# Performance work log

Hardware: AMD Instinct MI355X
Metric: run time of the kernel (lower is better)

Reference implementation:

```python
import jax, jax.numpy as jnp
import numpy as np

N_NODES = 50000
N_EDGES = 600000
H_DIM = 128
BN_EPS = 1e-5


def setup_inputs() -> dict:
    key = jax.random.key(0)
    k1, k2, k3, k4 = jax.random.split(key, 4)
    ent_emb = jax.random.normal(k1, (N_NODES, H_DIM), dtype=jnp.float32)
    # xavier_normal_ init for the 128x128 weight
    std = float(np.sqrt(2.0 / (H_DIM + H_DIM)))
    neigh_w = jax.random.normal(k2, (H_DIM, H_DIM), dtype=jnp.float32) * std
    gamma = jnp.ones((H_DIM,), dtype=jnp.float32)
    beta = jnp.zeros((H_DIM,), dtype=jnp.float32)
    src = jax.random.randint(k3, (N_EDGES,), 0, N_NODES, dtype=jnp.int32)
    dst = jax.random.randint(k4, (N_EDGES,), 0, N_NODES, dtype=jnp.int32)
    return {"ent_emb": ent_emb, "neigh_w": neigh_w, "gamma": gamma,
            "beta": beta, "src": src, "dst": dst}


def reference(ent_emb, neigh_w, gamma, beta, src, dst):
    # Edge dot-product scores: u_dot_v('emb','emb')  -> [E]
    e_src = ent_emb[src]                      # [E, H]
    e_dst = ent_emb[dst]                      # [E, H]
    scores = jnp.sum(e_src * e_dst, axis=-1)  # [E]

    # edge_softmax: softmax over incoming edges of each destination node
    seg_max = jax.ops.segment_max(scores, dst, num_segments=N_NODES)
    seg_max = jnp.where(jnp.isfinite(seg_max), seg_max, 0.0)  # nodes w/o edges
    e = jnp.exp(scores - seg_max[dst])                         # [E]
    seg_sum = jax.ops.segment_sum(e, dst, num_segments=N_NODES)
    norm = e / seg_sum[dst]                                    # [E]

    # update_all(u_mul_e, sum): weighted gather-sum aggregation
    msg = e_src * norm[:, None]                                # [E, H]
    neigh = jax.ops.segment_sum(msg, dst, num_segments=N_NODES)  # [N, H]

    # matmul + BatchNorm1d (training-mode batch stats) + tanh
    h = neigh @ neigh_w                                        # [N, H]
    mean = jnp.mean(h, axis=0)
    var = jnp.var(h, axis=0)  # biased, matches torch BN normalization
    h = (h - mean) * jax.lax.rsqrt(var + BN_EPS) * gamma + beta
    return jnp.tanh(h)
```

## Files before the change

kernel.cpp:

```cpp
#include <hip/hip_runtime.h>
#include <math.h>

#define N_NODES 50000
#define N_EDGES 600000
#define H 128
#define BN_EPS 1e-5f
#define MAXDEG 48

__global__ void k_scatter(const int* __restrict__ src, const int* __restrict__ dst,
                          int* __restrict__ cnt, int* __restrict__ slots) {
    int i = blockIdx.x * blockDim.x + threadIdx.x;
    if (i < N_EDGES) {
        int d = dst[i];
        int pos = atomicAdd(cnt + d, 1);
        if (pos < MAXDEG) slots[d * MAXDEG + pos] = src[i];
    }
}

#define F4SCALE(a, s) { (a).x *= (s); (a).y *= (s); (a).z *= (s); (a).w *= (s); }
#define F4FMA(a, e, v) { (a).x += (e)*(v).x; (a).y += (e)*(v).y; (a).z += (e)*(v).z; (a).w += (e)*(v).w; }
#define F4SHFLADD(a, msk) { (a).x += __shfl_xor((a).x, msk, 64); (a).y += __shfl_xor((a).y, msk, 64); \
                            (a).z += __shfl_xor((a).z, msk, 64); (a).w += __shfl_xor((a).w, msk, 64); }

__global__ __launch_bounds__(256) void k_fused(const float* __restrict__ emb,
                                               const int* __restrict__ cnt,
                                               const int* __restrict__ slots,
                                               float* __restrict__ neigh) {
    int wid = (blockIdx.x * blockDim.x + threadIdx.x) >> 6;
    int lane = threadIdx.x & 63;
    if (wid >= N_NODES) return;
    int g = lane >> 3;
    int l = lane & 7;

    int deg = min(cnt[wid], MAXDEG);
    int sid = slots[wid * MAXDEG + min(lane, MAXDEG - 1)];

    const float4* rd = (const float4*)(emb + (size_t)wid * H) + l * 4;
    float4 b0 = rd[0], b1 = rd[1], b2 = rd[2], b3 = rd[3];

    float m = -INFINITY, ssum = 0.0f;
    float4 acc0 = {0,0,0,0}, acc1 = {0,0,0,0}, acc2 = {0,0,0,0}, acc3 = {0,0,0,0};

    for (int cb = 0; cb < deg; cb += 8) {
        int e = cb + g;
        bool valid = e < deg;
        int s = __shfl(sid, valid ? e : 0, 64);
        const float4* rs = (const float4*)(emb + (size_t)s * H) + l * 4;
        float4 a0 = rs[0], a1 = rs[1], a2 = rs[2], a3 = rs[3];

        float v = a0.x*b0.x + a0.y*b0.y + a0.z*b0.z + a0.w*b0.w
                + a1.x*b1.x + a1.y*b1.y + a1.z*b1.z + a1.w*b1.w
                + a2.x*b2.x + a2.y*b2.y + a2.z*b2.z + a2.w*b2.w
                + a3.x*b3.x + a3.y*b3.y + a3.z*b3.z + a3.w*b3.w;
        v += __shfl_xor(v, 1, 64);
        v += __shfl_xor(v, 2, 64);
        v += __shfl_xor(v, 4, 64);
        if (!valid) v = -INFINITY;

        float cmax = v;
        cmax = fmaxf(cmax, __shfl_xor(cmax, 8, 64));
        cmax = fmaxf(cmax, __shfl_xor(cmax, 16, 64));
        cmax = fmaxf(cmax, __shfl_xor(cmax, 32, 64));
        float mnew = fmaxf(m, cmax);
        float scale = __expf(m - mnew);
        ssum *= scale;
        F4SCALE(acc0, scale); F4SCALE(acc1, scale);
        F4SCALE(acc2, scale); F4SCALE(acc3, scale);
        m = mnew;

        float ev = __expf(v - m);
        ssum += ev;
        F4FMA(acc0, ev, a0); F4FMA(acc1, ev, a1);
        F4FMA(acc2, ev, a2); F4FMA(acc3, ev, a3);
    }

    ssum += __shfl_xor(ssum, 8, 64);
    ssum += __shfl_xor(ssum, 16, 64);
    ssum += __shfl_xor(ssum, 32, 64);
    F4SHFLADD(acc0, 8);  F4SHFLADD(acc1, 8);  F4SHFLADD(acc2, 8);  F4SHFLADD(acc3, 8);
    F4SHFLADD(acc0, 16); F4SHFLADD(acc1, 16); F4SHFLADD(acc2, 16); F4SHFLADD(acc3, 16);
    F4SHFLADD(acc0, 32); F4SHFLADD(acc1, 32); F4SHFLADD(acc2, 32); F4SHFLADD(acc3, 32);

    float inv = (deg > 0) ? 1.0f / ssum : 0.0f;
    if (g == 0) {
        float4* po = (float4*)(neigh + (size_t)wid * H) + l * 4;
        F4SCALE(acc0, inv); F4SCALE(acc1, inv); F4SCALE(acc2, inv); F4SCALE(acc3, inv);
        po[0] = acc0; po[1] = acc1; po[2] = acc2; po[3] = acc3;
    }
}

#define MM_ROWS 128
#define MM_COLS 64
__global__ __launch_bounds__(256, 4) void k_matmul(const float* __restrict__ neigh,
                                                   const float* __restrict__ W,
                                                   float* __restrict__ hout,
                                                   float* __restrict__ stats) {
    __shared__ float Wl[H * MM_COLS];
    __shared__ float Sl[16 * MM_COLS];
    __shared__ float Ql[16 * MM_COLS];
    int t = threadIdx.x;
    int bc = blockIdx.x & 1;
    int br = blockIdx.x >> 1;
    int c0 = bc * MM_COLS;
    int n0 = br * MM_ROWS;
    int cg = t & 15, rg = t >> 4;
    int j0 = cg * 4;
    int r0 = n0 + rg * 8;

    for (int idx = t; idx < H * 16; idx += 256) {
        int k = idx >> 4, c4 = idx & 15;
        *(float4*)&Wl[k * MM_COLS + c4 * 4] =
            *((const float4*)(W + (size_t)k * H + c0) + c4);
    }

    const float* pr[8];
    bool valid[8];
#pragma unroll
    for (int i = 0; i < 8; ++i) {
        int n = r0 + i;
        valid[i] = (n < N_NODES);
        pr[i] = neigh + (size_t)(valid[i] ? n : 0) * H;
    }

    __syncthreads();

    float acc[8][4] = {};
    for (int k0 = 0; k0 < H; k0 += 4) {
        float4 rv[8];
#pragma unroll
        for (int i = 0; i < 8; ++i) rv[i] = *(const float4*)(pr[i] + k0);
        float4 wv[4];
#pragma unroll
        for (int kk = 0; kk < 4; ++kk) wv[kk] = *(const float4*)&Wl[(k0 + kk) * MM_COLS + j0];
#pragma unroll
        for (int kk = 0; kk < 4; ++kk) {
#pragma unroll
            for (int i = 0; i < 8; ++i) {
                float rk = ((const float*)&rv[i])[kk];
                acc[i][0] += rk * wv[kk].x;
                acc[i][1] += rk * wv[kk].y;
                acc[i][2] += rk * wv[kk].z;
                acc[i][3] += rk * wv[kk].w;
            }
        }
    }

#pragma unroll
    for (int i = 0; i < 8; ++i) {
        if (valid[i]) {
            float4 o = make_float4(acc[i][0], acc[i][1], acc[i][2], acc[i][3]);
            *(float4*)(hout + (size_t)(r0 + i) * H + c0 + j0) = o;
        }
    }

#pragma unroll
    for (int c = 0; c < 4; ++c) {
        float s = 0.0f, q = 0.0f;
#pragma unroll
        for (int i = 0; i < 8; ++i) {
            if (valid[i]) { s += acc[i][c]; q += acc[i][c] * acc[i][c]; }
        }
        Sl[rg * MM_COLS + j0 + c] = s;
        Ql[rg * MM_COLS + j0 + c] = q;
    }
    __syncthreads();
    if (t < MM_COLS) {
        float s = 0.0f;
#pragma unroll
        for (int r = 0; r < 16; ++r) s += Sl[r * MM_COLS + t];
        atomicAdd(stats + c0 + t, s);
    } else if (t < 2 * MM_COLS) {
        int j = t - MM_COLS;
        float q = 0.0f;
#pragma unroll
        for (int r = 0; r < 16; ++r) q += Ql[r * MM_COLS + j];
        atomicAdd(stats + 128 + c0 + j, q);
    }
}

__device__ __forceinline__ float tanh_fast(float x) {
    float e = __expf(2.0f * x);
    return 1.0f - 2.0f / (e + 1.0f);
}

__global__ __launch_bounds__(256) void k_apply(float* __restrict__ h,
                                               const float* __restrict__ stats,
                                               const float* __restrict__ gamma,
                                               const float* __restrict__ beta) {
    __shared__ float sc[128], sh[128];
    int t = threadIdx.x;
    if (t < 128) {
        float mean = stats[t] * (1.0f / N_NODES);
        float var = stats[128 + t] * (1.0f / N_NODES) - mean * mean;
        var = fmaxf(var, 0.0f);
        float s = gamma[t] * rsqrtf(var + BN_EPS);
        sc[t] = s;
        sh[t] = beta[t] - mean * s;
    }
    __syncthreads();
    int i = blockIdx.x * 256 + t;
    if (i < N_NODES * H / 4) {
        float4 v = ((const float4*)h)[i];
        int jb = (i & 31) * 4;
        v.x = tanh_fast(v.x * sc[jb]     + sh[jb]);
        v.y = tanh_fast(v.y * sc[jb + 1] + sh[jb + 1]);
        v.z = tanh_fast(v.z * sc[jb + 2] + sh[jb + 2]);
        v.w = tanh_fast(v.w * sc[jb + 3] + sh[jb + 3]);
        ((float4*)h)[i] = v;
    }
}

extern "C" void kernel_launch(void* const* d_in, const int* in_sizes, int n_in,
                              void* d_out, int out_size, void* d_ws, size_t ws_size,
                              hipStream_t stream) {
    const float* emb   = (const float*)d_in[0];
    const float* W     = (const float*)d_in[1];
    const float* gamma = (const float*)d_in[2];
    const float* beta  = (const float*)d_in[3];
    const int*   src   = (const int*)d_in[4];
    const int*   dst   = (const int*)d_in[5];
    float* out = (float*)d_out;

    int*   cnt   = (int*)d_ws;
    float* stats = (float*)(cnt + N_NODES);
    int*   slots = (int*)(stats + 256);
    float* neigh = (float*)(slots + (size_t)N_NODES * MAXDEG);

    hipMemsetAsync(cnt, 0, (N_NODES + 256) * sizeof(int), stream);
    k_scatter<<<(N_EDGES + 255) / 256, 256, 0, stream>>>(src, dst, cnt, slots);
    k_fused<<<(N_NODES * 64 + 255) / 256, 256, 0, stream>>>(emb, cnt, slots, neigh);
    k_matmul<<<((N_NODES + MM_ROWS - 1) / MM_ROWS) * 2, 256, 0, stream>>>(neigh, W, out, stats);
    k_apply<<<(N_NODES * H / 4 + 255) / 256, 256, 0, stream>>>(out, stats, gamma, beta);
}
```

Measured before the change: 218.8 us.

## Fuse BatchNorm apply into matmul via grid-wide barrier and skip redundant softmax rescale

The matmul kernel now keeps its output tile in registers, publishes per-column sum and sum-of-squares, then waits at an atomic grid-wide barrier before applying BatchNorm and tanh and writing the final output directly. This removes the separate apply kernel and its full read-modify-write pass over the 50000x128 output. The barrier relies on all 782 blocks being co-resident, which risks deadlock or spin stalls if occupancy assumptions fail. Separately, the online-softmax loop now skips the exp and accumulator rescale when the running max does not change.

```diff
diff --git a/kernel.cpp b/kernel.cpp
--- a/kernel.cpp
+++ b/kernel.cpp
@@ -62,11 +62,13 @@
         cmax = fmaxf(cmax, __shfl_xor(cmax, 16, 64));
         cmax = fmaxf(cmax, __shfl_xor(cmax, 32, 64));
         float mnew = fmaxf(m, cmax);
-        float scale = __expf(m - mnew);
-        ssum *= scale;
-        F4SCALE(acc0, scale); F4SCALE(acc1, scale);
-        F4SCALE(acc2, scale); F4SCALE(acc3, scale);
-        m = mnew;
+        if (mnew > m) {
+            float scale = __expf(m - mnew);
+            ssum *= scale;
+            F4SCALE(acc0, scale); F4SCALE(acc1, scale);
+            F4SCALE(acc2, scale); F4SCALE(acc3, scale);
+            m = mnew;
+        }
 
         float ev = __expf(v - m);
         ssum += ev;
@@ -89,15 +91,22 @@
     }
 }
 
+__device__ __forceinline__ float tanh_fast(float x) {
+    float e = __expf(2.0f * x);
+    return 1.0f - 2.0f / (e + 1.0f);
+}
+
 #define MM_ROWS 128
 #define MM_COLS 64
-__global__ __launch_bounds__(256, 4) void k_matmul(const float* __restrict__ neigh,
-                                                   const float* __restrict__ W,
-                                                   float* __restrict__ hout,
-                                                   float* __restrict__ stats) {
+#define NBLK (((N_NODES + MM_ROWS - 1) / MM_ROWS) * 2)
+__global__ __launch_bounds__(256, 4) void k_matmul_fused(const float* __restrict__ neigh,
+                                                         const float* __restrict__ W,
+                                                         float* __restrict__ out,
+                                                         float* __restrict__ stats,
+                                                         int* __restrict__ syncw,
+                                                         const float* __restrict__ gamma,
+                                                         const float* __restrict__ beta) {
     __shared__ float Wl[H * MM_COLS];
-    __shared__ float Sl[16 * MM_COLS];
-    __shared__ float Ql[16 * MM_COLS];
     int t = threadIdx.x;
     int bc = blockIdx.x & 1;
     int br = blockIdx.x >> 1;
@@ -145,14 +154,9 @@
         }
     }
 
-#pragma unroll
-    for (int i = 0; i < 8; ++i) {
-        if (valid[i]) {
-            float4 o = make_float4(acc[i][0], acc[i][1], acc[i][2], acc[i][3]);
-            *(float4*)(hout + (size_t)(r0 + i) * H + c0 + j0) = o;
-        }
-    }
-
+    __syncthreads();
+    float* Sl = Wl;
+    float* Ql = Wl + 16 * MM_COLS;
 #pragma unroll
     for (int c = 0; c < 4; ++c) {
         float s = 0.0f, q = 0.0f;
@@ -176,37 +180,53 @@
         for (int r = 0; r < 16; ++r) q += Ql[r * MM_COLS + j];
         atomicAdd(stats + 128 + c0 + j, q);
     }
-}
-
-__device__ __forceinline__ float tanh_fast(float x) {
-    float e = __expf(2.0f * x);
-    return 1.0f - 2.0f / (e + 1.0f);
-}
-
-__global__ __launch_bounds__(256) void k_apply(float* __restrict__ h,
-                                               const float* __restrict__ stats,
-                                               const float* __restrict__ gamma,
-                                               const float* __restrict__ beta) {
-    __shared__ float sc[128], sh[128];
-    int t = threadIdx.x;
-    if (t < 128) {
-        float mean = stats[t] * (1.0f / N_NODES);
-        float var = stats[128 + t] * (1.0f / N_NODES) - mean * mean;
-        var = fmaxf(var, 0.0f);
-        float s = gamma[t] * rsqrtf(var + BN_EPS);
-        sc[t] = s;
-        sh[t] = beta[t] - mean * s;
-    }
-    __syncthreads();
-    int i = blockIdx.x * 256 + t;
-    if (i < N_NODES * H / 4) {
-        float4 v = ((const float4*)h)[i];
-        int jb = (i & 31) * 4;
-        v.x = tanh_fast(v.x * sc[jb]     + sh[jb]);
-        v.y = tanh_fast(v.y * sc[jb + 1] + sh[jb + 1]);
-        v.z = tanh_fast(v.z * sc[jb + 2] + sh[jb + 2]);
-        v.w = tanh_fast(v.w * sc[jb + 3] + sh[jb + 3]);
-        ((float4*)h)[i] = v;
+
+    __threadfence();
+    __syncthreads();
+    if (t == 0) {
+        int old = __hip_atomic_fetch_add(&syncw[0], 1, __ATOMIC_ACQ_REL,
+                                         __HIP_MEMORY_SCOPE_AGENT);
+        if (old == NBLK - 1) {
+            __hip_atomic_store(&syncw[1], 1, __ATOMIC_RELEASE,
+                               __HIP_MEMORY_SCOPE_AGENT);
+        } else {
+            while (__hip_atomic_load(&syncw[1], __ATOMIC_ACQUIRE,
+                                     __HIP_MEMORY_SCOPE_AGENT) == 0) {
+                __builtin_amdgcn_s_sleep(8);
+            }
+        }
+    }
+    __syncthreads();
+
+    float sv[4], qv[4];
+#pragma unroll
+    for (int c = 0; c < 4; ++c) {
+        sv[c] = __hip_atomic_load(stats + c0 + j0 + c, __ATOMIC_RELAXED,
+                                  __HIP_MEMORY_SCOPE_AGENT);
+        qv[c] = __hip_atomic_load(stats + 128 + c0 + j0 + c, __ATOMIC_RELAXED,
+                                  __HIP_MEMORY_SCOPE_AGENT);
+    }
+    const float invN = 1.0f / N_NODES;
+    float sc[4], sh[4];
+#pragma unroll
+    for (int c = 0; c < 4; ++c) {
+        float mean = sv[c] * invN;
+        float var = fmaxf(qv[c] * invN - mean * mean, 0.0f);
+        float g2 = gamma[c0 + j0 + c];
+        float s = g2 * rsqrtf(var + BN_EPS);
+        sc[c] = s;
+        sh[c] = beta[c0 + j0 + c] - mean * s;
+    }
+#pragma unroll
+    for (int i = 0; i < 8; ++i) {
+        if (valid[i]) {
+            float4 o;
+            o.x = tanh_fast(acc[i][0] * sc[0] + sh[0]);
+            o.y = tanh_fast(acc[i][1] * sc[1] + sh[1]);
+            o.z = tanh_fast(acc[i][2] * sc[2] + sh[2]);
+            o.w = tanh_fast(acc[i][3] * sc[3] + sh[3]);
+            *(float4*)(out + (size_t)(r0 + i) * H + c0 + j0) = o;
+        }
     }
 }
 
@@ -223,12 +243,12 @@
 
     int*   cnt   = (int*)d_ws;
     float* stats = (float*)(cnt + N_NODES);
-    int*   slots = (int*)(stats + 256);
+    int*   syncw = (int*)(stats + 256);
+    int*   slots = syncw + 4;
     float* neigh = (float*)(slots + (size_t)N_NODES * MAXDEG);
 
-    hipMemsetAsync(cnt, 0, (N_NODES + 256) * sizeof(int), stream);
+    hipMemsetAsync(cnt, 0, (N_NODES + 260) * sizeof(int), stream);
     k_scatter<<<(N_EDGES + 255) / 256, 256, 0, stream>>>(src, dst, cnt, slots);
     k_fused<<<(N_NODES * 64 + 255) / 256, 256, 0, stream>>>(emb, cnt, slots, neigh);
-    k_matmul<<<((N_NODES + MM_ROWS - 1) / MM_ROWS) * 2, 256, 0, stream>>>(neigh, W, out, stats);
-    k_apply<<<(N_NODES * H / 4 + 255) / 256, 256, 0, stream>>>(out, stats, gamma, beta);
-}
+    k_matmul_fused<<<NBLK, 256, 0, stream>>>(neigh, W, out, stats, syncw, gamma, beta);
+}
```

Result: slower. 461.7 us (+111.0%).

## Store pre-BN matmul output as fp16 and skip redundant softmax rescales

Applied to the files above, without the earlier changes.

The matmul now writes its pre-normalization output to a half-precision scratch buffer, and a new apply kernel reads it and writes fp32 results. This halves the intermediate write and read traffic between the two kernels. BN statistics are still computed from the fp32 accumulators, but fp16 rounding of h adds error. The online softmax also skips the rescale of its accumulators when the running max does not increase. The fp16 path is used only if the workspace is large enough, otherwise the fp32 path runs.

```diff
diff --git a/kernel.cpp b/kernel.cpp
--- a/kernel.cpp
+++ b/kernel.cpp
@@ -1,4 +1,5 @@
 #include <hip/hip_runtime.h>
+#include <hip/hip_fp16.h>
 #include <math.h>
 
 #define N_NODES 50000
@@ -62,11 +63,13 @@
         cmax = fmaxf(cmax, __shfl_xor(cmax, 16, 64));
         cmax = fmaxf(cmax, __shfl_xor(cmax, 32, 64));
         float mnew = fmaxf(m, cmax);
-        float scale = __expf(m - mnew);
-        ssum *= scale;
-        F4SCALE(acc0, scale); F4SCALE(acc1, scale);
-        F4SCALE(acc2, scale); F4SCALE(acc3, scale);
-        m = mnew;
+        if (mnew > m) {
+            float scale = __expf(m - mnew);
+            ssum *= scale;
+            F4SCALE(acc0, scale); F4SCALE(acc1, scale);
+            F4SCALE(acc2, scale); F4SCALE(acc3, scale);
+            m = mnew;
+        }
 
         float ev = __expf(v - m);
         ssum += ev;
@@ -91,9 +94,11 @@
 
 #define MM_ROWS 128
 #define MM_COLS 64
+template <bool F16>
 __global__ __launch_bounds__(256, 4) void k_matmul(const float* __restrict__ neigh,
                                                    const float* __restrict__ W,
-                                                   float* __restrict__ hout,
+                                                   float* __restrict__ hout32,
+                                                   __half* __restrict__ hout16,
                                                    float* __restrict__ stats) {
     __shared__ float Wl[H * MM_COLS];
     __shared__ float Sl[16 * MM_COLS];
@@ -148,8 +153,15 @@
 #pragma unroll
     for (int i = 0; i < 8; ++i) {
         if (valid[i]) {
-            float4 o = make_float4(acc[i][0], acc[i][1], acc[i][2], acc[i][3]);
-            *(float4*)(hout + (size_t)(r0 + i) * H + c0 + j0) = o;
+            if (F16) {
+                __half2 h01 = __floats2half2_rn(acc[i][0], acc[i][1]);
+                __half2 h23 = __floats2half2_rn(acc[i][2], acc[i][3]);
+                __half2* p = (__half2*)(hout16 + (size_t)(r0 + i) * H + c0 + j0);
+                p[0] = h01; p[1] = h23;
+            } else {
+                float4 o = make_float4(acc[i][0], acc[i][1], acc[i][2], acc[i][3]);
+                *(float4*)(hout32 + (size_t)(r0 + i) * H + c0 + j0) = o;
+            }
         }
     }
 
@@ -183,10 +195,10 @@
     return 1.0f - 2.0f / (e + 1.0f);
 }
 
-__global__ __launch_bounds__(256) void k_apply(float* __restrict__ h,
-                                               const float* __restrict__ stats,
-                                               const float* __restrict__ gamma,
-                                               const float* __restrict__ beta) {
+__global__ __launch_bounds__(256) void k_apply_f32(float* __restrict__ h,
+                                                   const float* __restrict__ stats,
+                                                   const float* __restrict__ gamma,
+                                                   const float* __restrict__ beta) {
     __shared__ float sc[128], sh[128];
     int t = threadIdx.x;
     if (t < 128) {
@@ -207,6 +219,45 @@
         v.z = tanh_fast(v.z * sc[jb + 2] + sh[jb + 2]);
         v.w = tanh_fast(v.w * sc[jb + 3] + sh[jb + 3]);
         ((float4*)h)[i] = v;
+    }
+}
+
+__global__ __launch_bounds__(256) void k_apply_f16(const __half* __restrict__ h,
+                                                   float* __restrict__ out,
+                                                   const float* __restrict__ stats,
+                                                   const float* __restrict__ gamma,
+                                                   const float* __restrict__ beta) {
+    __shared__ float sc[128], sh[128];
+    int t = threadIdx.x;
+    if (t < 128) {
+        float mean = stats[t] * (1.0f / N_NODES);
+        float var = stats[128 + t] * (1.0f / N_NODES) - mean * mean;
+        var = fmaxf(var, 0.0f);
+        float s = gamma[t] * rsqrtf(var + BN_EPS);
+        sc[t] = s;
+        sh[t] = beta[t] - mean * s;
+    }
+    __syncthreads();
+    int i = blockIdx.x * 256 + t;
+    if (i < N_NODES * H / 8) {
+        union { uint4 u; __half2 h2[4]; } U;
+        U.u = ((const uint4*)h)[i];
+        int jb = (i & 15) * 8;
+        float2 f0 = __half22float2(U.h2[0]);
+        float2 f1 = __half22float2(U.h2[1]);
+        float2 f2 = __half22float2(U.h2[2]);
+        float2 f3 = __half22float2(U.h2[3]);
+        float4 o0, o1;
+        o0.x = tanh_fast(f0.x * sc[jb]     + sh[jb]);
+        o0.y = tanh_fast(f0.y * sc[jb + 1] + sh[jb + 1]);
+        o0.z = tanh_fast(f1.x * sc[jb + 2] + sh[jb + 2]);
+        o0.w = tanh_fast(f1.y * sc[jb + 3] + sh[jb + 3]);
+        o1.x = tanh_fast(f2.x * sc[jb + 4] + sh[jb + 4]);
+        o1.y = tanh_fast(f2.y * sc[jb + 5] + sh[jb + 5]);
+        o1.z = tanh_fast(f3.x * sc[jb + 6] + sh[jb + 6]);
+        o1.w = tanh_fast(f3.y * sc[jb + 7] + sh[jb + 7]);
+        ((float4*)out)[2 * i]     = o0;
+        ((float4*)out)[2 * i + 1] = o1;
     }
 }
 
@@ -221,14 +272,28 @@
     const int*   dst   = (const int*)d_in[5];
     float* out = (float*)d_out;
 
-    int*   cnt   = (int*)d_ws;
-    float* stats = (float*)(cnt + N_NODES);
-    int*   slots = (int*)(stats + 256);
-    float* neigh = (float*)(slots + (size_t)N_NODES * MAXDEG);
-
-    hipMemsetAsync(cnt, 0, (N_NODES + 256) * sizeof(int), stream);
+    int*    cnt   = (int*)d_ws;
+    float*  stats = (float*)(cnt + N_NODES);
+    int*    slots = (int*)(stats + 256) + 4;
+    float*  neigh = (float*)(slots + (size_t)N_NODES * MAXDEG);
+    __half* hbuf  = (__half*)(neigh + (size_t)N_NODES * H);
+
+    size_t need_f16 = (size_t)(N_NODES + 260) * 4
+                    + (size_t)N_NODES * MAXDEG * 4
+                    + (size_t)N_NODES * H * 4
+                    + (size_t)N_NODES * H * 2;
+    bool use_f16 = ws_size >= need_f16;
+
+    hipMemsetAsync(cnt, 0, (N_NODES + 260) * sizeof(int), stream);
     k_scatter<<<(N_EDGES + 255) / 256, 256, 0, stream>>>(src, dst, cnt, slots);
     k_fused<<<(N_NODES * 64 + 255) / 256, 256, 0, stream>>>(emb, cnt, slots, neigh);
-    k_matmul<<<((N_NODES + MM_ROWS - 1) / MM_ROWS) * 2, 256, 0, stream>>>(neigh, W, out, stats);
-    k_apply<<<(N_NODES * H / 4 + 255) / 256, 256, 0, stream>>>(out, stats, gamma, beta);
-}
+
+    int nblk_mm = ((N_NODES + MM_ROWS - 1) / MM_ROWS) * 2;
+    if (use_f16) {
+        k_matmul<true><<<nblk_mm, 256, 0, stream>>>(neigh, W, nullptr, hbuf, stats);
+        k_apply_f16<<<(N_NODES * H / 8 + 255) / 256, 256, 0, stream>>>(hbuf, out, stats, gamma, beta);
+    } else {
+        k_matmul<false><<<nblk_mm, 256, 0, stream>>>(neigh, W, out, nullptr, stats);
+        k_apply_f32<<<(N_NODES * H / 4 + 255) / 256, 256, 0, stream>>>(out, stats, gamma, beta);
+    }
+}
```

After: 217.5 us. Within noise of the previous version (-0.6%).
